# Kernel optimization log

Hardware: AMD Instinct MI355X
Metric: run time of the kernel (lower is better)

Reference implementation:

```python
import jax, jax.numpy as jnp
import numpy as np

B, I, K, O = 128, 64, 1024, 1024  # batch, kept in-axis, reduced in-axis, out-axis

def setup_inputs() -> dict:
    key = jax.random.key(0)
    k1, k2, k3 = jax.random.split(key, 3)
    stdv = 1.0 / np.sqrt(float(K))  # reduction covers in_shape[-1:] = [K]
    x = jax.random.normal(k1, (B, I, K), dtype=jnp.float32)
    weight = jax.random.uniform(k2, (O, I, K), dtype=jnp.float32, minval=-stdv, maxval=stdv)
    b = jax.random.uniform(k3, (O, I), dtype=jnp.float32, minval=-stdv, maxval=stdv)
    return {"x": x, "weight": weight, "b": b}

def reference(x, weight, b):
    # torch: unsqueeze x to [B,1,I,K], multiply by weight [O,I,K], sum last `reduction`=1
    # axes -> [B,O,I], add bias [O,I]. Expressed as a fused contraction:
    z = jnp.einsum('bik,oik->boi', x, weight)
    return z + b  # bias broadcasts over batch
```

## Files before the change

kernel.cpp:

```cpp
#include <hip/hip_runtime.h>

typedef __attribute__((ext_vector_type(8))) short  shortx8;
typedef __attribute__((ext_vector_type(4))) float  floatx4;

#define B_SZ 128
#define I_SZ 64
#define K_SZ 1024
#define O_SZ 1024
#define IK   (I_SZ * K_SZ)
#define OI   (O_SZ * I_SZ)
#define BK   32
#define NKT  (K_SZ / BK)

__device__ __forceinline__ unsigned short f2bf(float f) {
    unsigned int u = __builtin_bit_cast(unsigned int, f);
    u += 0x7fffu + ((u >> 16) & 1u);
    return (unsigned short)(u >> 16);
}

__device__ __forceinline__ shortx8 cvt8(float4 a, float4 b) {
    shortx8 r;
    r[0] = (short)f2bf(a.x); r[1] = (short)f2bf(a.y);
    r[2] = (short)f2bf(a.z); r[3] = (short)f2bf(a.w);
    r[4] = (short)f2bf(b.x); r[5] = (short)f2bf(b.y);
    r[6] = (short)f2bf(b.z); r[7] = (short)f2bf(b.w);
    return r;
}

__global__ __launch_bounds__(256, 2) void factlin_mfma(
    const float* __restrict__ x, const float* __restrict__ w,
    const float* __restrict__ bias, float* __restrict__ out)
{
    const int wg   = blockIdx.x;
    const int nt   = wg & 7;
    const int i    = wg >> 3;
    const int lane = threadIdx.x & 63;
    const int wid  = threadIdx.x >> 6;
    const int wm   = wid >> 1;
    const int wn   = wid & 1;
    const int lrow  = lane & 15;
    const int khalf = (lane >> 4) * 8;

    const float* ap = x + (wm * 64 + lrow) * IK + i * K_SZ + khalf;
    const float* bp = w + (nt * 128 + wn * 64 + lrow) * IK + i * K_SZ + khalf;

    float4 abuf[4][2];
    float4 bbuf[4][2];

    #pragma unroll
    for (int mi = 0; mi < 4; ++mi) {
        abuf[mi][0] = *(const float4*)(ap + mi * (16 * IK));
        abuf[mi][1] = *(const float4*)(ap + mi * (16 * IK) + 4);
        bbuf[mi][0] = *(const float4*)(bp + mi * (16 * IK));
        bbuf[mi][1] = *(const float4*)(bp + mi * (16 * IK) + 4);
    }

    floatx4 acc[4][4] = {};

    #pragma unroll 1
    for (int kt = 0; kt < NKT; ++kt) {
        shortx8 af[4], bf[4];
        #pragma unroll
        for (int mi = 0; mi < 4; ++mi) af[mi] = cvt8(abuf[mi][0], abuf[mi][1]);
        #pragma unroll
        for (int ni = 0; ni < 4; ++ni) bf[ni] = cvt8(bbuf[ni][0], bbuf[ni][1]);

        if (kt + 1 < NKT) {
            const float* ap2 = ap + (kt + 1) * BK;
            const float* bp2 = bp + (kt + 1) * BK;
            #pragma unroll
            for (int mi = 0; mi < 4; ++mi) {
                abuf[mi][0] = *(const float4*)(ap2 + mi * (16 * IK));
                abuf[mi][1] = *(const float4*)(ap2 + mi * (16 * IK) + 4);
                bbuf[mi][0] = *(const float4*)(bp2 + mi * (16 * IK));
                bbuf[mi][1] = *(const float4*)(bp2 + mi * (16 * IK) + 4);
            }
        }

        #pragma unroll
        for (int mi = 0; mi < 4; ++mi)
            #pragma unroll
            for (int ni = 0; ni < 4; ++ni)
                acc[mi][ni] = __builtin_amdgcn_mfma_f32_16x16x32_bf16(
                    af[mi], bf[ni], acc[mi][ni], 0, 0, 0);
    }

    const int obase = nt * 128 + wn * 64;
    float bv[4];
    #pragma unroll
    for (int ni = 0; ni < 4; ++ni)
        bv[ni] = bias[(obase + ni * 16 + lrow) * I_SZ + i];

    const int rb = wm * 64 + (lane >> 4) * 4;
    #pragma unroll
    for (int mi = 0; mi < 4; ++mi) {
        #pragma unroll
        for (int ni = 0; ni < 4; ++ni) {
            const int ocol = obase + ni * 16 + lrow;
            float* op = out + (rb + mi * 16) * OI + ocol * I_SZ + i;
            #pragma unroll
            for (int r = 0; r < 4; ++r)
                op[r * OI] = acc[mi][ni][r] + bv[ni];
        }
    }
}

extern "C" void kernel_launch(void* const* d_in, const int* in_sizes, int n_in,
                              void* d_out, int out_size, void* d_ws, size_t ws_size,
                              hipStream_t stream) {
    const float* x  = (const float*)d_in[0];
    const float* w  = (const float*)d_in[1];
    const float* b  = (const float*)d_in[2];
    float* out      = (float*)d_out;

    factlin_mfma<<<dim3(512), dim3(256), 0, stream>>>(x, w, b, out);
}
```

Measured before the change: 457.9 us.

## Stage bf16-converted A/B tiles in swizzled LDS with wider K tile

Replaces the register-direct per-wave global loads with a cooperative load of 128x128 fp32 tiles for A and B. Each tile is converted to bf16 and stored in XOR-swizzled shared memory, then read back by the MFMA loop. Every element is now loaded and converted once per workgroup instead of redundantly by each wave, and the rows are read as contiguous 512-byte segments. The cost is two barriers per K step and no software prefetch across steps, so global latency is exposed. The 64KB of LDS may also limit occupancy.

```diff
diff --git a/kernel.cpp b/kernel.cpp
--- a/kernel.cpp
+++ b/kernel.cpp
@@ -1,16 +1,16 @@
 #include <hip/hip_runtime.h>
 
 typedef __attribute__((ext_vector_type(8))) short  shortx8;
+typedef __attribute__((ext_vector_type(4))) short  shortx4;
 typedef __attribute__((ext_vector_type(4))) float  floatx4;
 
-#define B_SZ 128
 #define I_SZ 64
 #define K_SZ 1024
-#define O_SZ 1024
-#define IK   (I_SZ * K_SZ)
-#define OI   (O_SZ * I_SZ)
-#define BK   32
+#define IK   65536
+#define OI   65536
+#define BK   128
 #define NKT  (K_SZ / BK)
+#define LROW 256
 
 __device__ __forceinline__ unsigned short f2bf(float f) {
     unsigned int u = __builtin_bit_cast(unsigned int, f);
@@ -18,71 +18,96 @@
     return (unsigned short)(u >> 16);
 }
 
-__device__ __forceinline__ shortx8 cvt8(float4 a, float4 b) {
-    shortx8 r;
+__device__ __forceinline__ shortx4 cvt4(float4 a) {
+    shortx4 r;
     r[0] = (short)f2bf(a.x); r[1] = (short)f2bf(a.y);
     r[2] = (short)f2bf(a.z); r[3] = (short)f2bf(a.w);
-    r[4] = (short)f2bf(b.x); r[5] = (short)f2bf(b.y);
-    r[6] = (short)f2bf(b.z); r[7] = (short)f2bf(b.w);
     return r;
 }
 
-__global__ __launch_bounds__(256, 2) void factlin_mfma(
+__global__ __launch_bounds__(256, 2) void factlin_mfma2(
     const float* __restrict__ x, const float* __restrict__ w,
     const float* __restrict__ bias, float* __restrict__ out)
 {
+    __shared__ __align__(16) char lA[128 * LROW];
+    __shared__ __align__(16) char lB[128 * LROW];
+
     const int wg   = blockIdx.x;
     const int nt   = wg & 7;
     const int i    = wg >> 3;
-    const int lane = threadIdx.x & 63;
-    const int wid  = threadIdx.x >> 6;
+    const int tid  = threadIdx.x;
+    const int lane = tid & 63;
+    const int wid  = tid >> 6;
     const int wm   = wid >> 1;
     const int wn   = wid & 1;
-    const int lrow  = lane & 15;
-    const int khalf = (lane >> 4) * 8;
+    const int lrow = lane & 15;
+    const int g    = lane >> 4;
 
-    const float* ap = x + (wm * 64 + lrow) * IK + i * K_SZ + khalf;
-    const float* bp = w + (nt * 128 + wn * 64 + lrow) * IK + i * K_SZ + khalf;
-
-    float4 abuf[4][2];
-    float4 bbuf[4][2];
-
-    #pragma unroll
-    for (int mi = 0; mi < 4; ++mi) {
-        abuf[mi][0] = *(const float4*)(ap + mi * (16 * IK));
-        abuf[mi][1] = *(const float4*)(ap + mi * (16 * IK) + 4);
-        bbuf[mi][0] = *(const float4*)(bp + mi * (16 * IK));
-        bbuf[mi][1] = *(const float4*)(bp + mi * (16 * IK) + 4);
-    }
+    const float* gA = x + i * K_SZ;
+    const float* gB = w + (nt * 128) * IK + i * K_SZ;
 
     floatx4 acc[4][4] = {};
 
     #pragma unroll 1
     for (int kt = 0; kt < NKT; ++kt) {
-        shortx8 af[4], bf[4];
+        __syncthreads();
+
+        float4 buf[8];
         #pragma unroll
-        for (int mi = 0; mi < 4; ++mi) af[mi] = cvt8(abuf[mi][0], abuf[mi][1]);
+        for (int grp = 0; grp < 2; ++grp) {
+            #pragma unroll
+            for (int e = 0; e < 8; ++e) {
+                const int c = (grp * 8 + e) * 256 + tid;
+                buf[e] = *(const float4*)(gA + (c >> 5) * IK + kt * BK + (c & 31) * 4);
+            }
+            #pragma unroll
+            for (int e = 0; e < 8; ++e) {
+                const int c = (grp * 8 + e) * 256 + tid;
+                const int row = c >> 5;
+                const int off = row * LROW + (((c & 31) * 8) ^ ((row & 7) << 4));
+                *(shortx4*)(lA + off) = cvt4(buf[e]);
+            }
+        }
         #pragma unroll
-        for (int ni = 0; ni < 4; ++ni) bf[ni] = cvt8(bbuf[ni][0], bbuf[ni][1]);
-
-        if (kt + 1 < NKT) {
-            const float* ap2 = ap + (kt + 1) * BK;
-            const float* bp2 = bp + (kt + 1) * BK;
+        for (int grp = 0; grp < 2; ++grp) {
             #pragma unroll
-            for (int mi = 0; mi < 4; ++mi) {
-                abuf[mi][0] = *(const float4*)(ap2 + mi * (16 * IK));
-                abuf[mi][1] = *(const float4*)(ap2 + mi * (16 * IK) + 4);
-                bbuf[mi][0] = *(const float4*)(bp2 + mi * (16 * IK));
-                bbuf[mi][1] = *(const float4*)(bp2 + mi * (16 * IK) + 4);
+            for (int e = 0; e < 8; ++e) {
+                const int c = (grp * 8 + e) * 256 + tid;
+                buf[e] = *(const float4*)(gB + (c >> 5) * IK + kt * BK + (c & 31) * 4);
+            }
+            #pragma unroll
+            for (int e = 0; e < 8; ++e) {
+                const int c = (grp * 8 + e) * 256 + tid;
+                const int row = c >> 5;
+                const int off = row * LROW + (((c & 31) * 8) ^ ((row & 7) << 4));
+                *(shortx4*)(lB + off) = cvt4(buf[e]);
             }
         }
 
+        __syncthreads();
+
         #pragma unroll
-        for (int mi = 0; mi < 4; ++mi)
+        for (int ks = 0; ks < 4; ++ks) {
+            shortx8 af[4], bf[4];
             #pragma unroll
-            for (int ni = 0; ni < 4; ++ni)
-                acc[mi][ni] = __builtin_amdgcn_mfma_f32_16x16x32_bf16(
-                    af[mi], bf[ni], acc[mi][ni], 0, 0, 0);
+            for (int mi = 0; mi < 4; ++mi) {
+                const int row = wm * 64 + mi * 16 + lrow;
+                const int off = row * LROW + ((ks * 64 + g * 16) ^ ((row & 7) << 4));
+                af[mi] = *(const shortx8*)(lA + off);
+            }
+            #pragma unroll
+            for (int ni = 0; ni < 4; ++ni) {
+                const int row = wn * 64 + ni * 16 + lrow;
+                const int off = row * LROW + ((ks * 64 + g * 16) ^ ((row & 7) << 4));
+                bf[ni] = *(const shortx8*)(lB + off);
+            }
+            #pragma unroll
+            for (int mi = 0; mi < 4; ++mi)
+                #pragma unroll
+                for (int ni = 0; ni < 4; ++ni)
+                    acc[mi][ni] = __builtin_amdgcn_mfma_f32_16x16x32_bf16(
+                        af[mi], bf[ni], acc[mi][ni], 0, 0, 0);
+        }
     }
 
     const int obase = nt * 128 + wn * 64;
@@ -91,7 +116,7 @@
     for (int ni = 0; ni < 4; ++ni)
         bv[ni] = bias[(obase + ni * 16 + lrow) * I_SZ + i];
 
-    const int rb = wm * 64 + (lane >> 4) * 4;
+    const int rb = wm * 64 + g * 4;
     #pragma unroll
     for (int mi = 0; mi < 4; ++mi) {
         #pragma unroll
@@ -113,5 +138,5 @@
     const float* b  = (const float*)d_in[2];
     float* out      = (float*)d_out;
 
-    factlin_mfma<<<dim3(512), dim3(256), 0, stream>>>(x, w, b, out);
+    factlin_mfma2<<<dim3(512), dim3(256), 0, stream>>>(x, w, b, out);
 }
```

Result: slower. 523.5 us (+14.3%).
